# Kernel tuning notes

Hardware: AMD Instinct MI355X
Metric: run time of the kernel (lower is better)

The kernel has to match this reference:

```python
import jax, jax.numpy as jnp
import numpy as np
from functools import partial

N_SEEDS = 1000       # n
BG_LOW, BG_UP = 0.3, 0.7
ERODE_K, ERODE_ITER = 11, 1
KSZ = 3
IGNORE = -255
INT_MAX = np.iinfo(np.int32).max


def _min_pool2d(x, k):
    # binary erosion with a kxk all-ones structuring element, SAME padding
    return jax.lax.reduce_window(x, INT_MAX, jax.lax.min, (k, k), (1, 1), 'SAME')


def _max_pool3d(x, k):
    # binary dilation over (B,H,W) with kxk window on spatial dims
    return jax.lax.reduce_window(x, -INT_MAX, jax.lax.max, (1, k, k), (1, 1, 1), 'SAME')


def _otsu_threshold(flat255):
    # flat255: int32 pixel values in [0,255]
    hist = jnp.zeros(256, jnp.float32).at[flat255].add(1.0)
    total = jnp.asarray(flat255.shape[0], jnp.float32)
    bins = jnp.arange(256, dtype=jnp.float32)
    w = jnp.cumsum(hist)                 # class-0 pixel count up to bin t
    m = jnp.cumsum(hist * bins)          # class-0 intensity mass up to t
    mT = m[-1]
    denom = w * (total - w)
    sigma_b = jnp.where(denom > 0, (mT * w - total * m) ** 2 / (denom * total * total), 0.0)
    th = jnp.argmax(sigma_b).astype(jnp.float32)
    bad = jnp.sum(hist > 0) <= 1         # degenerate histogram -> bad_egg
    return th, bad


def _sample_mask(eligible, key, hw):
    # uniform sampling without replacement of min(N_SEEDS, #eligible)
    # via random-score top-k restricted to eligible positions
    scores = jnp.where(eligible, jax.random.uniform(key, (hw,)), -jnp.inf)
    vals, idx = jax.lax.top_k(scores, N_SEEDS)
    sel = (vals > -jnp.inf).astype(jnp.int32)
    return jnp.zeros(hw, jnp.int32).at[idx].max(sel)


def _one_sample(cam, key):
    h, w = cam.shape
    hw = h * w
    cam255 = jnp.floor(cam * 255.0)
    flat255 = jnp.clip(cam255.astype(jnp.int32).ravel(), 0, 255)

    th, bad = _otsu_threshold(flat255)
    th = jnp.where(bad, jnp.median(cam * 255.0), th)
    th = jnp.where(th == 0, 1.0, jnp.where(th == 255, 254.0, th))

    roi = (cam255 > th).astype(jnp.int32)
    for _ in range(ERODE_ITER):
        roi = _min_pool2d(roi, ERODE_K)

    kf, kb, kz = jax.random.split(key, 3)
    # foreground: sample uniformly from eroded ROI pixels
    fg = _sample_mask(roi.ravel() == 1, kf, hw)
    # background: sample uniformly from the nbr_bg lowest-activation pixels
    z = jax.random.uniform(kz, (), minval=BG_LOW, maxval=BG_UP)
    nbr_bg = jnp.ceil(z * hw)
    order = jnp.argsort(cam.ravel())
    rank = jnp.zeros(hw, jnp.int32).at[order].set(jnp.arange(hw, dtype=jnp.int32))
    bg = _sample_mask(rank.astype(jnp.float32) < nbr_bg, kb, hw)
    return fg.reshape(h, w), bg.reshape(h, w)


def setup_inputs() -> dict:
    key = jax.random.key(0)
    x = jax.random.uniform(key, (128, 1, 512, 512), dtype=jnp.float32)
    return {"x": x}


def reference(x):
    b, d, h, w = x.shape
    keys = jax.random.split(jax.random.key(42), b)
    all_fg, all_bg = jax.vmap(_one_sample)(x[:, 0], keys)   # (B,H,W) int32
    # dilation with ksz x ksz ones kernel
    all_fg = _max_pool3d(all_fg, KSZ)
    all_bg = _max_pool3d(all_bg, KSZ)
    outer = all_fg + all_bg
    all_fg = jnp.where(outer == 2, 0, all_fg)
    all_bg = jnp.where(outer == 2, 0, all_bg)
    out = jnp.full((b, h, w), IGNORE, dtype=jnp.int32)
    out = jnp.where(all_fg == 1, 1, out)
    out = jnp.where(all_bg == 1, 0, out)
    return out
```

## Files before the change

### kernel.cpp

```cpp
#include <hip/hip_runtime.h>
#include <cstdint>

typedef unsigned short u16;

constexpr int BATCH = 128;
constexpr int H = 512, W = 512;
constexpr int HW = H * W;
constexpr int WPR = W / 64;
constexpr int WPI = HW / 64;
constexpr int NSEED = 1000;
constexpr int MARGIN = 3000;
constexpr int CAP2 = 4096;
constexpr int CAPS = 1024;
constexpr int LBUF = 2048;
constexpr int NBIN = 4096;
constexpr int QSEG = 576;

__device__ __forceinline__ uint32_t rotl32(uint32_t v, int d) {
  return (v << d) | (v >> (32 - d));
}

__device__ __forceinline__ void tf2x32(uint32_t k0, uint32_t k1,
                                       uint32_t x0, uint32_t x1,
                                       uint32_t &o0, uint32_t &o1) {
  uint32_t ks2 = k0 ^ k1 ^ 0x1BD11BDAu;
  x0 += k0; x1 += k1;
  x0 += x1; x1 = rotl32(x1, 13); x1 ^= x0;
  x0 += x1; x1 = rotl32(x1, 15); x1 ^= x0;
  x0 += x1; x1 = rotl32(x1, 26); x1 ^= x0;
  x0 += x1; x1 = rotl32(x1, 6);  x1 ^= x0;
  x0 += k1; x1 += ks2 + 1u;
  x0 += x1; x1 = rotl32(x1, 17); x1 ^= x0;
  x0 += x1; x1 = rotl32(x1, 29); x1 ^= x0;
  x0 += x1; x1 = rotl32(x1, 16); x1 ^= x0;
  x0 += x1; x1 = rotl32(x1, 24); x1 ^= x0;
  x0 += ks2; x1 += k0 + 2u;
  x0 += x1; x1 = rotl32(x1, 13); x1 ^= x0;
  x0 += x1; x1 = rotl32(x1, 15); x1 ^= x0;
  x0 += x1; x1 = rotl32(x1, 26); x1 ^= x0;
  x0 += x1; x1 = rotl32(x1, 6);  x1 ^= x0;
  x0 += k0; x1 += k1 + 3u;
  x0 += x1; x1 = rotl32(x1, 17); x1 ^= x0;
  x0 += x1; x1 = rotl32(x1, 29); x1 ^= x0;
  x0 += x1; x1 = rotl32(x1, 16); x1 ^= x0;
  x0 += x1; x1 = rotl32(x1, 24); x1 ^= x0;
  x0 += k1; x1 += ks2 + 4u;
  x0 += x1; x1 = rotl32(x1, 13); x1 ^= x0;
  x0 += x1; x1 = rotl32(x1, 15); x1 ^= x0;
  x0 += x1; x1 = rotl32(x1, 26); x1 ^= x0;
  x0 += x1; x1 = rotl32(x1, 6);  x1 ^= x0;
  x0 += ks2; x1 += k0 + 5u;
  o0 = x0; o1 = x1;
}

__device__ __forceinline__ uint32_t score_bits(uint32_t k0, uint32_t k1, uint32_t i) {
  uint32_t a, c; tf2x32(k0, k1, 0u, i, a, c);
  return a ^ c;
}

__device__ __forceinline__ void keygen(int b, uint32_t* keys, uint32_t* kbg,
                                       uint32_t* Tbg) {
  uint32_t kb0, kb1; tf2x32(0u, 42u, 0u, (uint32_t)b, kb0, kb1);
  uint32_t kf0, kf1; tf2x32(kb0, kb1, 0u, 0u, kf0, kf1);
  uint32_t kB0, kB1; tf2x32(kb0, kb1, 0u, 1u, kB0, kB1);
  uint32_t kz0, kz1; tf2x32(kb0, kb1, 0u, 2u, kz0, kz1);
  uint32_t za, zc; tf2x32(kz0, kz1, 0u, 0u, za, zc);
  uint32_t zb = za ^ zc;
  keys[b * 4 + 0] = kf0; keys[b * 4 + 1] = kf1;
  keys[b * 4 + 2] = kB0; keys[b * 4 + 3] = kB1;
  float uu = __uint_as_float((zb >> 9) | 0x3f800000u) - 1.0f;
  float span = __fsub_rn(0.7f, 0.3f);
  float z = __fadd_rn(__fmul_rn(uu, span), 0.3f);
  z = fmaxf(0.3f, z);
  float nb = ceilf(__fmul_rn(z, (float)HW));
  uint32_t K = (uint32_t)nb;
  kbg[b] = K;
  float tv = floorf((1.0f - (float)MARGIN / (float)K) * 8388608.0f);
  Tbg[b] = (uint32_t)fmaxf(tv, 0.0f);
}

__global__ __launch_bounds__(1024) void k_binify(const float4* __restrict__ x4,
                                                 u16* __restrict__ g,
                                                 uint32_t* __restrict__ gh,
                                                 uint32_t* __restrict__ keys,
                                                 uint32_t* __restrict__ kbg,
                                                 uint32_t* __restrict__ Tbg,
                                                 uint32_t* __restrict__ Efg,
                                                 uint32_t* __restrict__ cnt_fg,
                                                 uint32_t* __restrict__ cnt_be,
                                                 uint32_t* __restrict__ cnt_bg) {
  __shared__ uint32_t h[NBIN];
  int b = blockIdx.x >> 2, sub = blockIdx.x & 3, t = threadIdx.x;
  if (blockIdx.x == 0 && t < BATCH) {
    keygen(t, keys, kbg, Tbg);
    Efg[t] = 0; cnt_fg[t] = 0; cnt_be[t] = 0; cnt_bg[t] = 0;
  }
  for (int i = t; i < NBIN; i += 1024) h[i] = 0;
  __syncthreads();
  const float4* xb = x4 + ((size_t)b * HW + (size_t)sub * (HW / 4)) / 4;
  ushort4* gb4 = (ushort4*)g + ((size_t)b * HW + (size_t)sub * (HW / 4)) / 4;
  for (int i = t; i < HW / 16; i += 1024) {
    float4 v4 = xb[i];
    int g0 = (int)floorf(__fmul_rn(v4.x, 4080.0f)); g0 = min(max(g0, 0), 4079);
    int g1 = (int)floorf(__fmul_rn(v4.y, 4080.0f)); g1 = min(max(g1, 0), 4079);
    int g2 = (int)floorf(__fmul_rn(v4.z, 4080.0f)); g2 = min(max(g2, 0), 4079);
    int g3 = (int)floorf(__fmul_rn(v4.w, 4080.0f)); g3 = min(max(g3, 0), 4079);
    atomicAdd(&h[g0], 1u);
    atomicAdd(&h[g1], 1u);
    atomicAdd(&h[g2], 1u);
    atomicAdd(&h[g3], 1u);
    ushort4 o;
    o.x = (u16)g0; o.y = (u16)g1; o.z = (u16)g2; o.w = (u16)g3;
    gb4[i] = o;
  }
  __syncthreads();
  uint32_t* dst = gh + ((size_t)blockIdx.x << 12);
  for (int i = t; i < NBIN; i += 1024) dst[i] = h[i];
}

__device__ __forceinline__ void lds_tree_cumsum256(float* L, float* S, int tid) {
  const int off[9] = {0, 256, 384, 448, 480, 496, 504, 508, 510};
  const int sz[9]  = {256, 128, 64, 32, 16, 8, 4, 2, 1};
  for (int l = 0; l < 8; ++l) {
    int o = off[l], on = off[l + 1], n = sz[l + 1];
    if (tid < n) L[on + tid] = __fadd_rn(L[o + 2 * tid], L[o + 2 * tid + 1]);
    __syncthreads();
  }
  if (tid == 0) S[off[8]] = L[off[8]];
  __syncthreads();
  for (int l = 7; l >= 0; --l) {
    int o = off[l], on = off[l + 1], hn = sz[l] / 2;
    if (tid == 0) S[o] = L[o];
    if (tid < hn) S[o + 2 * tid + 1] = S[on + tid];
    if (tid >= 1 && tid < hn) S[o + 2 * tid] = __fadd_rn(S[on + tid - 1], L[o + 2 * tid]);
    __syncthreads();
  }
}

__global__ __launch_bounds__(256) void k_otsu_scan(const uint32_t* __restrict__ gh,
                                                   const uint32_t* __restrict__ Ka,
                                                   int* __restrict__ th_out,
                                                   uint32_t* __restrict__ b1a,
                                                   uint32_t* __restrict__ r1a) {
  __shared__ float L[511], S[511], wc[256], mm[256];
  __shared__ float sv[256];
  __shared__ int si[256];
  __shared__ uint32_t h[NBIN];
  __shared__ uint32_t ps[256];
  int tid = threadIdx.x;
  int b = (blockIdx.x < BATCH) ? blockIdx.x : (blockIdx.x - BATCH);
  const uint32_t* g0 = gh + ((size_t)(b * 4 + 0) << 12);
  const uint32_t* g1 = gh + ((size_t)(b * 4 + 1) << 12);
  const uint32_t* g2 = gh + ((size_t)(b * 4 + 2) << 12);
  const uint32_t* g3 = gh + ((size_t)(b * 4 + 3) << 12);
  for (int i = tid; i < NBIN; i += 256) h[i] = g0[i] + g1[i] + g2[i] + g3[i];
  __syncthreads();
  if (blockIdx.x < BATCH) {
    uint32_t hv = 0;
#pragma unroll
    for (int i = 0; i < 16; ++i) hv += h[tid * 16 + i];
    L[tid] = (float)hv;
    __syncthreads();
    lds_tree_cumsum256(L, S, tid);
    wc[tid] = S[tid];
    __syncthreads();
    L[tid] = __fmul_rn((float)hv, (float)tid);
    __syncthreads();
    lds_tree_cumsum256(L, S, tid);
    mm[tid] = S[tid];
    __syncthreads();
    float total = (float)HW;
    float mT = mm[255];
    {
      float w = wc[tid];
      float denom = __fmul_rn(w, __fsub_rn(total, w));
      float s = 0.0f;
      if (denom > 0.0f) {
        float d  = __fsub_rn(__fmul_rn(mT, w), __fmul_rn(total, mm[tid]));
        float nu = __fmul_rn(d, d);
        float dd = __fmul_rn(__fmul_rn(denom, total), total);
        s = __fdiv_rn(nu, dd);
      }
      sv[tid] = s; si[tid] = tid;
    }
    __syncthreads();
    for (int st = 128; st >= 1; st >>= 1) {
      if (tid < st) {
        float s2 = sv[tid + st]; int i2 = si[tid + st];
        if (s2 > sv[tid] || (s2 == sv[tid] && i2 < si[tid])) { sv[tid] = s2; si[tid] = i2; }
      }
      __syncthreads();
    }
    if (tid == 0) {
      int bi = si[0];
      if (bi == 0) bi = 1;
      if (bi == 255) bi = 254;
      th_out[b] = bi;
    }
  } else {
    uint32_t K = Ka[b];
    uint32_t s = 0;
#pragma unroll
    for (int i = 0; i < 16; ++i) s += h[tid * 16 + i];
    ps[tid] = s;
    __syncthreads();
    if (tid == 0) {
      uint32_t acc = 0, b1 = 0, r1 = 1;
      for (int c = 0; c < 256; ++c) {
        if (acc + ps[c] >= K) {
          for (int bin = c * 16; bin < c * 16 + 16; ++bin) {
            uint32_t cc = h[bin];
            if (acc + cc >= K) { b1 = (uint32_t)bin; r1 = K - acc; break; }
            acc += cc;
          }
          break;
        }
        acc += ps[c];
      }
      b1a[b] = b1; r1a[b] = r1;
    }
  }
}

__global__ __launch_bounds__(1024) void k_main(const u16* __restrict__ gq,
                                               const float* __restrict__ x,
                                               const int* __restrict__ th,
                                               const uint32_t* __restrict__ b1a,
                                               const uint32_t* __restrict__ Tbg,
                                               const uint32_t* __restrict__ keys,
                                               uint32_t* __restrict__ Efg,
                                               uint32_t* __restrict__ cnt_bg,
                                               uint64_t* __restrict__ list,
                                               uint32_t* __restrict__ cnt_be,
                                               uint64_t* __restrict__ list_be,
                                               uint64_t* __restrict__ erod) {
  __shared__ uint64_t sroi[1104];
  __shared__ uint64_t srow[1104];
  __shared__ uint32_t wq[16 * QSEG];
  __shared__ uint64_t lbuf[LBUF];
  __shared__ uint32_t lcnt, gbase;
  int b = blockIdx.x >> 2, sub = blockIdx.x & 3, t = threadIdx.x;
  int wave = t >> 6, lane = t & 63;
  int R0 = sub * 128;
  int rlo = max(R0 - 5, 0), rhi = min(R0 + 133, H);
  int nwords = (rhi - rlo) * 8;
  const u16* gb = gq + (size_t)b * HW;
  const float* xb = x + (size_t)b * HW;
  int groi = (th[b] + 1) << 4;
  uint32_t b1 = b1a[b];
  uint32_t T = Tbg[b];
  uint32_t k0 = keys[b * 4 + 2], k1 = keys[b * 4 + 3];
  if (t == 0) lcnt = 0;
  __syncthreads();
  uint32_t* q = wq + wave * QSEG;
  uint32_t qlen = 0, hd = 0;
  uint64_t lmask = (1ull << lane) - 1ull;
  for (int r = 0; r < 8; ++r) {
    int absr = R0 + wave * 8 + r;
    int rowbase = absr * W + lane;
    int swbase = (absr - rlo) * 8;
    const u16* gp8 = gb + rowbase;
    u16 gvals[8];
#pragma unroll
    for (int c = 0; c < 8; ++c) gvals[c] = gp8[c * 64];
#pragma unroll
    for (int c = 0; c < 8; ++c) {
      uint32_t gv = (uint32_t)gvals[c];
      uint64_t bw = __ballot((int)gv >= groi);
      if (lane == 0) sroi[swbase + c] = bw;
      bool elig = gv < b1;
      uint64_t m = __ballot(elig);
      if (elig) {
        uint32_t rank = (uint32_t)__popcll(m & lmask);
        uint32_t idx = hd + qlen + rank;
        if (idx >= (uint32_t)QSEG) idx -= (uint32_t)QSEG;
        q[idx] = (uint32_t)(rowbase + c * 64);
      }
      qlen += (uint32_t)__popcll(m);
      if (gv == b1) {
        uint32_t gp = atomicAdd(&cnt_be[b], 1u);
        if (gp < (uint32_t)CAPS)
          list_be[(size_t)b * CAPS + gp] =
              (((uint64_t)__float_as_uint(xb[rowbase + c * 64])) << 18) |
              (uint32_t)(rowbase + c * 64);
      }
    }
    while (qlen >= 64u) {
      __builtin_amdgcn_wave_barrier();
      uint32_t idx = hd + (uint32_t)lane;
      if (idx >= (uint32_t)QSEG) idx -= (uint32_t)QSEG;
      uint32_t p = q[idx];
      hd += 64u; if (hd >= (uint32_t)QSEG) hd -= (uint32_t)QSEG;
      qlen -= 64u;
      uint32_t v = score_bits(k0, k1, p) >> 9;
      if (v >= T) {
        uint32_t pos = atomicAdd(&lcnt, 1u);
        uint64_t key = (((uint64_t)((~v) & 0x7FFFFFu)) << 18) | p;
        if (pos < (uint32_t)LBUF) lbuf[pos] = key;
        else { uint32_t gp = atomicAdd(&cnt_bg[b], 1u);
               if (gp < (uint32_t)CAP2) list[(size_t)b * CAP2 + gp] = key; }
      }
    }
  }
  if (qlen) {
    __builtin_amdgcn_wave_barrier();
    if ((uint32_t)lane < qlen) {
      uint32_t idx = hd + (uint32_t)lane;
      if (idx >= (uint32_t)QSEG) idx -= (uint32_t)QSEG;
      uint32_t p = q[idx];
      uint32_t v = score_bits(k0, k1, p) >> 9;
      if (v >= T) {
        uint32_t pos = atomicAdd(&lcnt, 1u);
        uint64_t key = (((uint64_t)((~v) & 0x7FFFFFu)) << 18) | p;
        if (pos < (uint32_t)LBUF) lbuf[pos] = key;
        else { uint32_t gp = atomicAdd(&cnt_bg[b], 1u);
               if (gp < (uint32_t)CAP2) list[(size_t)b * CAP2 + gp] = key; }
      }
    }
  }
  {
    int lowWords = (R0 - rlo) * 8;
    int nh = nwords - 1024;
    for (int i = wave; i < nh; i += 16) {
      int wi = i + ((i < lowWords) ? 0 : 1024);
      int absr = rlo + (wi >> 3);
      int c = wi & 7;
      uint32_t gv = (uint32_t)gb[absr * W + c * 64 + lane];
      uint64_t bw = __ballot((int)gv >= groi);
      if (lane == 0) sroi[wi] = bw;
    }
  }
  __syncthreads();
  for (int wi = t; wi < nwords; wi += 1024) {
    int c = wi & 7;
    uint64_t cur = sroi[wi];
    uint64_t left  = (c > 0) ? sroi[wi - 1] : ~0ull;
    uint64_t right = (c < 7) ? sroi[wi + 1] : ~0ull;
    uint64_t res = cur;
#pragma unroll
    for (int s = 1; s <= 5; ++s) {
      res &= (cur >> s) | (right << (64 - s));
      res &= (cur << s) | (left >> (64 - s));
    }
    srow[wi] = res;
  }
  __syncthreads();
  {
    int coreRow = t >> 3, c = t & 7;
    int absr = R0 + coreRow;
    int s = absr - rlo;
    uint64_t res = srow[s * 8 + c];
#pragma unroll
    for (int d = 1; d <= 5; ++d) {
      if (absr - d >= 0) res &= srow[(s - d) * 8 + c];
      if (absr + d < H)  res &= srow[(s + d) * 8 + c];
    }
    erod[(size_t)b * WPI + absr * 8 + c] = res;
    uint32_t pc = (uint32_t)__popcll(res);
    for (int sh = 32; sh >= 1; sh >>= 1) pc += __shfl_down(pc, sh);
    if (lane == 0 && pc) atomicAdd(&Efg[b], pc);
  }
  __syncthreads();
  int m = min((int)lcnt, LBUF);
  if (t == 0) gbase = atomicAdd(&cnt_bg[b], (uint32_t)m);
  __syncthreads();
  uint32_t base = gbase;
  for (int i = t; i < m; i += 1024) {
    uint32_t pos = base + (uint32_t)i;
    if (pos < (uint32_t)CAP2) list[(size_t)b * CAP2 + pos] = lbuf[i];
  }
}

__global__ __launch_bounds__(1024) void k_select(const uint32_t* __restrict__ r1a,
                                                 const uint32_t* __restrict__ cnt_be,
                                                 const uint64_t* __restrict__ list_be,
                                                 const uint32_t* __restrict__ Tbg,
                                                 const uint32_t* __restrict__ keys,
                                                 const uint32_t* __restrict__ cnt_bg,
                                                 const uint64_t* __restrict__ list,
                                                 uint64_t* __restrict__ bmG,
                                                 const uint32_t* __restrict__ Ea,
                                                 uint32_t* __restrict__ cnt_fg,
                                                 uint64_t* __restrict__ list_fg,
                                                 const uint64_t* __restrict__ bmE,
                                                 uint64_t* __restrict__ bmF) {
  __shared__ uint64_t pool[5248];
  __shared__ uint32_t ecnt, tcnt, lcnt, gbase, sb2, sr2;
  int t = threadIdx.x;
  uint32_t* h = (uint32_t*)(pool + 2048);
  uint64_t* tie = pool + 4096;
  uint32_t* S = (uint32_t*)(pool + 5120);
  if (blockIdx.x < BATCH) {
    int b = blockIdx.x;
    uint64_t* ks = pool;
    uint64_t* ebuf = pool + 1024;
    uint64_t* bg = bmG + (size_t)b * WPI;
    for (int i = t; i < WPI; i += 1024) bg[i] = 0;
    int nbe = min((int)cnt_be[b], CAPS);
    if (t == 0) { ecnt = 0; tcnt = 0; }
    if (t < nbe) ks[t] = list_be[(size_t)b * CAPS + t];
    __syncthreads();
    if (t < nbe) {
      uint64_t mk = ks[t];
      int rank = 0;
      for (int i = 0; i < nbe; ++i) rank += (ks[i] < mk) ? 1 : 0;
      int r = min((int)r1a[b], nbe);
      if (rank < r) {
        uint32_t p = (uint32_t)(mk & 0x3FFFFull);
        uint32_t v = score_bits(keys[b * 4 + 2], keys[b * 4 + 3], p) >> 9;
        if (v >= Tbg[b]) {
          uint32_t slot = atomicAdd(&ecnt, 1u);
          ebuf[slot] = (((uint64_t)((~v) & 0x7FFFFFu)) << 18) | p;
        }
      }
    }
    for (int i = t; i < 4096; i += 1024) h[i] = 0;
    __syncthreads();
    int n0 = min((int)cnt_bg[b], CAP2);
    int ne = (int)ecnt;
    int n = n0 + ne;
    if (n == 0) return;
    uint32_t target = (uint32_t)min(NSEED, n);
    const uint64_t* lb = list + (size_t)b * CAP2;
    uint64_t K0 = (t < n0)        ? lb[t]        : 0;
    uint64_t K1 = (t + 1024 < n0) ? lb[t + 1024] : 0;
    uint64_t K2 = (t + 2048 < n0) ? lb[t + 2048] : 0;
    uint64_t K3 = (t + 3072 < n0) ? lb[t + 3072] : 0;
    uint64_t KE = (t < ne)        ? ebuf[t]      : 0;
    if (t < n0)        atomicAdd(&h[(uint32_t)(K0 >> 29)], 1u);
    if (t + 1024 < n0) atomicAdd(&h[(uint32_t)(K1 >> 29)], 1u);
    if (t + 2048 < n0) atomicAdd(&h[(uint32_t)(K2 >> 29)], 1u);
    if (t + 3072 < n0) atomicAdd(&h[(uint32_t)(K3 >> 29)], 1u);
    if (t < ne)        atomicAdd(&h[(uint32_t)(KE >> 29)], 1u);
    __syncthreads();
    if (t < 256) {
      uint32_t s = 0;
#pragma unroll
      for (int i = 0; i < 16; ++i) s += h[t * 16 + i];
      S[t] = s;
    }
    __syncthreads();
    for (int st = 1; st < 256; st <<= 1) {
      uint32_t v = 0;
      if (t < 256 && t >= st) v = S[t - st];
      __syncthreads();
      if (t < 256) S[t] += v;
      __syncthreads();
    }
    if (t < 256) {
      uint32_t before = (t == 0) ? 0u : S[t - 1];
      if (S[t] >= target && before < target) {
        uint32_t acc = before;
        for (int i = 0; i < 16; ++i) {
          uint32_t c = h[t * 16 + i];
          if (acc + c >= target) { sb2 = (uint32_t)(t * 16 + i); sr2 = target - acc; break; }
          acc += c;
        }
      }
    }
    __syncthreads();
    uint32_t b2 = sb2, r2 = sr2;
#define PROC(KK, VALID) \
    if (VALID) { \
      uint32_t bin = (uint32_t)((KK) >> 29); \
      if (bin < b2) { \
        uint32_t p = (uint32_t)(KK) & 0x3FFFFu; \
        atomicOr((unsigned long long*)&bg[p >> 6], 1ull << (p & 63)); \
      } else if (bin == b2) { \
        uint32_t pos = atomicAdd(&tcnt, 1u); \
        if (pos < 1024u) tie[pos] = (KK); \
      } \
    }
    PROC(K0, t < n0) PROC(K1, t + 1024 < n0) PROC(K2, t + 2048 < n0)
    PROC(K3, t + 3072 < n0) PROC(KE, t < ne)
#undef PROC
    __syncthreads();
    int m = min((int)tcnt, 1024);
    int r = min((int)r2, m);
    if (t < m) {
      uint64_t mk = tie[t];
      int rank = 0;
      for (int i = 0; i < m; ++i) rank += (tie[i] < mk) ? 1 : 0;
      if (rank < r) {
        uint32_t p = (uint32_t)mk & 0x3FFFFu;
        atomicOr((unsigned long long*)&bg[p >> 6], 1ull << (p & 63));
      }
    }
  } else {
    int b = blockIdx.x - BATCH;
    uint32_t E = Ea[b];
    if (E <= (uint32_t)NSEED) return;
    uint64_t* lbuf = pool;
    const uint64_t* eb = bmE + (size_t)b * WPI;
    uint64_t* ob = bmF + (size_t)b * WPI;
    for (int i = t; i < WPI; i += 1024) ob[i] = 0;
    if (t == 0) { lcnt = 0; tcnt = 0; }
    __syncthreads();
    float tvf = floorf((1.0f - (float)MARGIN / (float)E) * 8388608.0f);
    uint32_t T = (uint32_t)fmaxf(tvf, 0.0f);
    uint32_t k0 = keys[b * 4 + 0], k1 = keys[b * 4 + 1];
    int lane = t & 63;
    for (int k = 0; k < HW / 1024; ++k) {
      uint32_t p = (uint32_t)(k * 1024 + t);
      uint64_t wbits = eb[p >> 6];
      if ((wbits >> lane) & 1ull) {
        uint32_t v = score_bits(k0, k1, p) >> 9;
        if (v >= T) {
          uint32_t pos = atomicAdd(&lcnt, 1u);
          uint64_t key = (((uint64_t)((~v) & 0x7FFFFFu)) << 18) | p;
          if (pos < (uint32_t)LBUF) lbuf[pos] = key;
          else { uint32_t gp = atomicAdd(&cnt_fg[b], 1u);
                 if (gp < (uint32_t)CAP2) list_fg[(size_t)b * CAP2 + gp] = key; }
        }
      }
    }
    __syncthreads();
    int m2 = min((int)lcnt, LBUF);
    if (t == 0) gbase = atomicAdd(&cnt_fg[b], (uint32_t)m2);
    __syncthreads();
    for (int i = t; i < m2; i += 1024) {
      uint32_t pos = gbase + (uint32_t)i;
      if (pos < (uint32_t)CAP2) list_fg[(size_t)b * CAP2 + pos] = lbuf[i];
    }
    __syncthreads();
    int n = min((int)cnt_fg[b], CAP2);
    if (n == 0) return;
    uint32_t target = (uint32_t)min(NSEED, n);
    const uint64_t* lb = list_fg + (size_t)b * CAP2;
    uint64_t K0 = (t < n)        ? lb[t]        : 0;
    uint64_t K1 = (t + 1024 < n) ? lb[t + 1024] : 0;
    uint64_t K2 = (t + 2048 < n) ? lb[t + 2048] : 0;
    uint64_t K3 = (t + 3072 < n) ? lb[t + 3072] : 0;
    for (int i = t; i < 4096; i += 1024) h[i] = 0;
    __syncthreads();
    if (t < n)        atomicAdd(&h[(uint32_t)(K0 >> 29)], 1u);
    if (t + 1024 < n) atomicAdd(&h[(uint32_t)(K1 >> 29)], 1u);
    if (t + 2048 < n) atomicAdd(&h[(uint32_t)(K2 >> 29)], 1u);
    if (t + 3072 < n) atomicAdd(&h[(uint32_t)(K3 >> 29)], 1u);
    __syncthreads();
    if (t < 256) {
      uint32_t s = 0;
#pragma unroll
      for (int i = 0; i < 16; ++i) s += h[t * 16 + i];
      S[t] = s;
    }
    __syncthreads();
    for (int st = 1; st < 256; st <<= 1) {
      uint32_t v = 0;
      if (t < 256 && t >= st) v = S[t - st];
      __syncthreads();
      if (t < 256) S[t] += v;
      __syncthreads();
    }
    if (t < 256) {
      uint32_t before = (t == 0) ? 0u : S[t - 1];
      if (S[t] >= target && before < target) {
        uint32_t acc = before;
        for (int i = 0; i < 16; ++i) {
          uint32_t c = h[t * 16 + i];
          if (acc + c >= target) { sb2 = (uint32_t)(t * 16 + i); sr2 = target - acc; break; }
          acc += c;
        }
      }
    }
    __syncthreads();
    uint32_t b2 = sb2, r2 = sr2;
#define PROC(KK, VALID) \
    if (VALID) { \
      uint32_t bin = (uint32_t)((KK) >> 29); \
      if (bin < b2) { \
        uint32_t p = (uint32_t)(KK) & 0x3FFFFu; \
        atomicOr((unsigned long long*)&ob[p >> 6], 1ull << (p & 63)); \
      } else if (bin == b2) { \
        uint32_t pos = atomicAdd(&tcnt, 1u); \
        if (pos < 1024u) tie[pos] = (KK); \
      } \
    }
    PROC(K0, t < n) PROC(K1, t + 1024 < n) PROC(K2, t + 2048 < n) PROC(K3, t + 3072 < n)
#undef PROC
    __syncthreads();
    int m = min((int)tcnt, 1024);
    int r = min((int)r2, m);
    if (t < m) {
      uint64_t mk = tie[t];
      int rank = 0;
      for (int i = 0; i < m; ++i) rank += (tie[i] < mk) ? 1 : 0;
      if (rank < r) {
        uint32_t p = (uint32_t)mk & 0x3FFFFu;
        atomicOr((unsigned long long*)&ob[p >> 6], 1ull << (p & 63));
      }
    }
  }
}

__global__ __launch_bounds__(256) void k_compose4(const uint64_t* __restrict__ bmE,
                                                  const uint64_t* __restrict__ bmF,
                                                  const uint64_t* __restrict__ G,
                                                  const uint32_t* __restrict__ Ea,
                                                  int* __restrict__ out) {
  int tid = blockIdx.x * 256 + threadIdx.x;
  int w = tid >> 4;
  int sub = tid & 15;
  int iw = w & (WPI - 1);
  int b = w >> 12;
  const uint64_t* F = (Ea[b] <= (uint32_t)NSEED) ? bmE : bmF;
  int r = iw >> 3, c = iw & 7;
  int ib = w - iw;
  uint64_t Fd = 0, Bd = 0;
#pragma unroll
  for (int dr = -1; dr <= 1; ++dr) {
    int rr = r + dr;
    if (rr < 0 || rr >= H) continue;
    int wi = ib + rr * 8 + c;
    uint64_t cf = F[wi], cg = G[wi];
    uint64_t lf = (c > 0) ? F[wi - 1] : 0ull, lg = (c > 0) ? G[wi - 1] : 0ull;
    uint64_t rf = (c < 7) ? F[wi + 1] : 0ull, rg = (c < 7) ? G[wi + 1] : 0ull;
    Fd |= cf | (cf << 1) | (lf >> 63) | (cf >> 1) | (rf << 63);
    Bd |= cg | (cg << 1) | (lg >> 63) | (cg >> 1) | (rg << 63);
  }
  uint64_t ov = Fd & Bd;
  Fd &= ~ov; Bd &= ~ov;
  int sh = sub * 4;
  int4 o;
  o.x = ((Fd >> (sh + 0)) & 1ull) ? 1 : (((Bd >> (sh + 0)) & 1ull) ? 0 : -255);
  o.y = ((Fd >> (sh + 1)) & 1ull) ? 1 : (((Bd >> (sh + 1)) & 1ull) ? 0 : -255);
  o.z = ((Fd >> (sh + 2)) & 1ull) ? 1 : (((Bd >> (sh + 2)) & 1ull) ? 0 : -255);
  o.w = ((Fd >> (sh + 3)) & 1ull) ? 1 : (((Bd >> (sh + 3)) & 1ull) ? 0 : -255);
  ((int4*)out)[tid] = o;
}

extern "C" void kernel_launch(void* const* d_in, const int* in_sizes, int n_in,
                              void* d_out, int out_size, void* d_ws, size_t ws_size,
                              hipStream_t stream) {
  (void)in_sizes; (void)n_in; (void)out_size; (void)ws_size;
  const float* x = (const float*)d_in[0];
  int* out = (int*)d_out;
  char* ws = (char*)d_ws;

  u16* g = (u16*)d_out;

  uint32_t* keys   = (uint32_t*)(ws + 0);
  uint32_t* kbg    = (uint32_t*)(ws + 2048);
  int*      th     = (int*)     (ws + 2560);
  uint32_t* b1be   = (uint32_t*)(ws + 3072);
  uint32_t* r1be   = (uint32_t*)(ws + 3584);
  uint32_t* Tbg    = (uint32_t*)(ws + 4096);
  uint32_t* Efg    = (uint32_t*)(ws + 4608);
  uint32_t* cnt_fg = (uint32_t*)(ws + 5120);
  uint32_t* cnt_be = (uint32_t*)(ws + 5632);
  uint32_t* cnt_bg = (uint32_t*)(ws + 6144);
  char* P = ws + 8192;
  uint32_t* gh      = (uint32_t*)(P);
  uint64_t* bmG     = (uint64_t*)(P + 8396800 - 8192);
  uint64_t* _bmG    = (uint64_t*)(ws + 8192 + 8388608);
  uint64_t* list    = (uint64_t*)(ws + 8192 + 8388608 + 4194304);
  uint64_t* list_be = (uint64_t*)(ws + 8192 + 8388608 + 8388608);
  uint64_t* bmE     = (uint64_t*)(ws + 8192 + 8388608 + 9437184);
  uint64_t* bmF     = (uint64_t*)(ws + 8192 + 8388608 + 13631488);
  uint64_t* list_fg = (uint64_t*)gh;
  (void)bmG;

  k_binify   <<<BATCH * 4, 1024, 0, stream>>>((const float4*)x, g, gh, keys, kbg,
                                              Tbg, Efg, cnt_fg, cnt_be, cnt_bg);
  k_otsu_scan<<<BATCH * 2, 256, 0, stream>>>(gh, kbg, th, b1be, r1be);
  k_main     <<<BATCH * 4, 1024, 0, stream>>>(g, x, th, b1be, Tbg, keys,
                                              Efg, cnt_bg, list, cnt_be, list_be, bmE);
  k_select   <<<BATCH * 2, 1024, 0, stream>>>(r1be, cnt_be, list_be, Tbg, keys,
                                              cnt_bg, list, _bmG,
                                              Efg, cnt_fg, list_fg, bmE, bmF);
  k_compose4 <<<(BATCH * HW / 4) / 256, 256, 0, stream>>>(bmE, bmF, _bmG, Efg, out);
}
```

Before: 388.8 us.

## Fuse Otsu/background-scan into main kernel and stage dilation bitmaps in LDS

Removes the separate k_otsu_scan launch. Each k_main block now sums the four partial histograms, computes the Otsu threshold and the background bin cutoff itself, and keeps them in LDS through a union that shares space with the ROI buffers. This gets rid of one kernel launch and the global round trip for the threshold values, at the cost of every one of the four sub-blocks per image repeating the histogram work. Separately, the compose kernel now computes the dilated F/B words once per 8-row group into shared memory and writes the outputs from there. Before, every output thread reloaded up to nine bitmap words.

```diff
diff --git a/kernel.cpp b/kernel.cpp
--- a/kernel.cpp
+++ b/kernel.cpp
@@ -137,121 +137,120 @@
   }
 }
 
-__global__ __launch_bounds__(256) void k_otsu_scan(const uint32_t* __restrict__ gh,
-                                                   const uint32_t* __restrict__ Ka,
-                                                   int* __restrict__ th_out,
-                                                   uint32_t* __restrict__ b1a,
-                                                   uint32_t* __restrict__ r1a) {
-  __shared__ float L[511], S[511], wc[256], mm[256];
-  __shared__ float sv[256];
-  __shared__ int si[256];
-  __shared__ uint32_t h[NBIN];
-  __shared__ uint32_t ps[256];
-  int tid = threadIdx.x;
-  int b = (blockIdx.x < BATCH) ? blockIdx.x : (blockIdx.x - BATCH);
-  const uint32_t* g0 = gh + ((size_t)(b * 4 + 0) << 12);
-  const uint32_t* g1 = gh + ((size_t)(b * 4 + 1) << 12);
-  const uint32_t* g2 = gh + ((size_t)(b * 4 + 2) << 12);
-  const uint32_t* g3 = gh + ((size_t)(b * 4 + 3) << 12);
-  for (int i = tid; i < NBIN; i += 256) h[i] = g0[i] + g1[i] + g2[i] + g3[i];
-  __syncthreads();
-  if (blockIdx.x < BATCH) {
-    uint32_t hv = 0;
-#pragma unroll
-    for (int i = 0; i < 16; ++i) hv += h[tid * 16 + i];
-    L[tid] = (float)hv;
-    __syncthreads();
-    lds_tree_cumsum256(L, S, tid);
-    wc[tid] = S[tid];
-    __syncthreads();
-    L[tid] = __fmul_rn((float)hv, (float)tid);
-    __syncthreads();
-    lds_tree_cumsum256(L, S, tid);
-    mm[tid] = S[tid];
-    __syncthreads();
-    float total = (float)HW;
-    float mT = mm[255];
-    {
-      float w = wc[tid];
-      float denom = __fmul_rn(w, __fsub_rn(total, w));
-      float s = 0.0f;
-      if (denom > 0.0f) {
-        float d  = __fsub_rn(__fmul_rn(mT, w), __fmul_rn(total, mm[tid]));
-        float nu = __fmul_rn(d, d);
-        float dd = __fmul_rn(__fmul_rn(denom, total), total);
-        s = __fdiv_rn(nu, dd);
-      }
-      sv[tid] = s; si[tid] = tid;
-    }
-    __syncthreads();
-    for (int st = 128; st >= 1; st >>= 1) {
-      if (tid < st) {
-        float s2 = sv[tid + st]; int i2 = si[tid + st];
-        if (s2 > sv[tid] || (s2 == sv[tid] && i2 < si[tid])) { sv[tid] = s2; si[tid] = i2; }
-      }
-      __syncthreads();
-    }
-    if (tid == 0) {
-      int bi = si[0];
-      if (bi == 0) bi = 1;
-      if (bi == 255) bi = 254;
-      th_out[b] = bi;
-    }
-  } else {
-    uint32_t K = Ka[b];
-    uint32_t s = 0;
-#pragma unroll
-    for (int i = 0; i < 16; ++i) s += h[tid * 16 + i];
-    ps[tid] = s;
-    __syncthreads();
-    if (tid == 0) {
-      uint32_t acc = 0, b1 = 0, r1 = 1;
-      for (int c = 0; c < 256; ++c) {
-        if (acc + ps[c] >= K) {
-          for (int bin = c * 16; bin < c * 16 + 16; ++bin) {
-            uint32_t cc = h[bin];
-            if (acc + cc >= K) { b1 = (uint32_t)bin; r1 = K - acc; break; }
-            acc += cc;
-          }
-          break;
-        }
-        acc += ps[c];
-      }
-      b1a[b] = b1; r1a[b] = r1;
-    }
-  }
-}
-
 __global__ __launch_bounds__(1024) void k_main(const u16* __restrict__ gq,
                                                const float* __restrict__ x,
-                                               const int* __restrict__ th,
-                                               const uint32_t* __restrict__ b1a,
+                                               const uint32_t* __restrict__ gh,
+                                               const uint32_t* __restrict__ kbg,
                                                const uint32_t* __restrict__ Tbg,
                                                const uint32_t* __restrict__ keys,
+                                               uint32_t* __restrict__ r1a,
                                                uint32_t* __restrict__ Efg,
                                                uint32_t* __restrict__ cnt_bg,
                                                uint64_t* __restrict__ list,
                                                uint32_t* __restrict__ cnt_be,
                                                uint64_t* __restrict__ list_be,
                                                uint64_t* __restrict__ erod) {
-  __shared__ uint64_t sroi[1104];
-  __shared__ uint64_t srow[1104];
+  __shared__ union {
+    struct { uint64_t sroi[1104]; uint64_t srow[1104]; } m;
+    struct { uint32_t h[NBIN]; float L[511]; float S[511];
+             float wc[256]; float mm[256]; float sv[256];
+             int si[256]; uint32_t ps[256]; } o;
+  } u;
   __shared__ uint32_t wq[16 * QSEG];
   __shared__ uint64_t lbuf[LBUF];
   __shared__ uint32_t lcnt, gbase;
+  __shared__ int thS;
+  __shared__ uint32_t b1S;
   int b = blockIdx.x >> 2, sub = blockIdx.x & 3, t = threadIdx.x;
   int wave = t >> 6, lane = t & 63;
+
+  {
+    const uint32_t* g0 = gh + ((size_t)(b * 4 + 0) << 12);
+    const uint32_t* g1 = gh + ((size_t)(b * 4 + 1) << 12);
+    const uint32_t* g2 = gh + ((size_t)(b * 4 + 2) << 12);
+    const uint32_t* g3 = gh + ((size_t)(b * 4 + 3) << 12);
+    for (int i = t; i < NBIN; i += 1024) u.o.h[i] = g0[i] + g1[i] + g2[i] + g3[i];
+    __syncthreads();
+    uint32_t hv = 0;
+    if (t < 256) {
+#pragma unroll
+      for (int i = 0; i < 16; ++i) hv += u.o.h[t * 16 + i];
+      u.o.L[t] = (float)hv;
+    }
+    __syncthreads();
+    lds_tree_cumsum256(u.o.L, u.o.S, t);
+    if (t < 256) u.o.wc[t] = u.o.S[t];
+    __syncthreads();
+    if (t < 256) u.o.L[t] = __fmul_rn((float)hv, (float)t);
+    __syncthreads();
+    lds_tree_cumsum256(u.o.L, u.o.S, t);
+    if (t < 256) u.o.mm[t] = u.o.S[t];
+    __syncthreads();
+    if (t < 256) {
+      float total = (float)HW;
+      float mT = u.o.mm[255];
+      float w = u.o.wc[t];
+      float denom = __fmul_rn(w, __fsub_rn(total, w));
+      float s = 0.0f;
+      if (denom > 0.0f) {
+        float d  = __fsub_rn(__fmul_rn(mT, w), __fmul_rn(total, u.o.mm[t]));
+        float nu = __fmul_rn(d, d);
+        float dd = __fmul_rn(__fmul_rn(denom, total), total);
+        s = __fdiv_rn(nu, dd);
+      }
+      u.o.sv[t] = s; u.o.si[t] = t;
+    }
+    __syncthreads();
+    for (int st = 128; st >= 1; st >>= 1) {
+      if (t < st) {
+        float s2 = u.o.sv[t + st]; int i2 = u.o.si[t + st];
+        if (s2 > u.o.sv[t] || (s2 == u.o.sv[t] && i2 < u.o.si[t])) {
+          u.o.sv[t] = s2; u.o.si[t] = i2;
+        }
+      }
+      __syncthreads();
+    }
+    if (t < 256) {
+      uint32_t s = 0;
+#pragma unroll
+      for (int i = 0; i < 16; ++i) s += u.o.h[t * 16 + i];
+      u.o.ps[t] = s;
+    }
+    __syncthreads();
+    if (t == 0) {
+      int bi = u.o.si[0];
+      if (bi == 0) bi = 1;
+      if (bi == 255) bi = 254;
+      thS = bi;
+      uint32_t K = kbg[b];
+      uint32_t acc = 0, b1 = 0, r1 = 1;
+      for (int c = 0; c < 256; ++c) {
+        if (acc + u.o.ps[c] >= K) {
+          for (int bin = c * 16; bin < c * 16 + 16; ++bin) {
+            uint32_t cc = u.o.h[bin];
+            if (acc + cc >= K) { b1 = (uint32_t)bin; r1 = K - acc; break; }
+            acc += cc;
+          }
+          break;
+        }
+        acc += u.o.ps[c];
+      }
+      b1S = b1;
+      if (sub == 0) r1a[b] = r1;
+      lcnt = 0;
+    }
+    __syncthreads();
+  }
+
   int R0 = sub * 128;
   int rlo = max(R0 - 5, 0), rhi = min(R0 + 133, H);
   int nwords = (rhi - rlo) * 8;
   const u16* gb = gq + (size_t)b * HW;
   const float* xb = x + (size_t)b * HW;
-  int groi = (th[b] + 1) << 4;
-  uint32_t b1 = b1a[b];
+  int groi = (thS + 1) << 4;
+  uint32_t b1 = b1S;
   uint32_t T = Tbg[b];
   uint32_t k0 = keys[b * 4 + 2], k1 = keys[b * 4 + 3];
-  if (t == 0) lcnt = 0;
-  __syncthreads();
   uint32_t* q = wq + wave * QSEG;
   uint32_t qlen = 0, hd = 0;
   uint64_t lmask = (1ull << lane) - 1ull;
@@ -267,7 +266,7 @@
     for (int c = 0; c < 8; ++c) {
       uint32_t gv = (uint32_t)gvals[c];
       uint64_t bw = __ballot((int)gv >= groi);
-      if (lane == 0) sroi[swbase + c] = bw;
+      if (lane == 0) u.m.sroi[swbase + c] = bw;
       bool elig = gv < b1;
       uint64_t m = __ballot(elig);
       if (elig) {
@@ -327,33 +326,33 @@
       int c = wi & 7;
       uint32_t gv = (uint32_t)gb[absr * W + c * 64 + lane];
       uint64_t bw = __ballot((int)gv >= groi);
-      if (lane == 0) sroi[wi] = bw;
+      if (lane == 0) u.m.sroi[wi] = bw;
     }
   }
   __syncthreads();
   for (int wi = t; wi < nwords; wi += 1024) {
     int c = wi & 7;
-    uint64_t cur = sroi[wi];
-    uint64_t left  = (c > 0) ? sroi[wi - 1] : ~0ull;
-    uint64_t right = (c < 7) ? sroi[wi + 1] : ~0ull;
+    uint64_t cur = u.m.sroi[wi];
+    uint64_t left  = (c > 0) ? u.m.sroi[wi - 1] : ~0ull;
+    uint64_t right = (c < 7) ? u.m.sroi[wi + 1] : ~0ull;
     uint64_t res = cur;
 #pragma unroll
     for (int s = 1; s <= 5; ++s) {
       res &= (cur >> s) | (right << (64 - s));
       res &= (cur << s) | (left >> (64 - s));
     }
-    srow[wi] = res;
+    u.m.srow[wi] = res;
   }
   __syncthreads();
   {
     int coreRow = t >> 3, c = t & 7;
     int absr = R0 + coreRow;
     int s = absr - rlo;
-    uint64_t res = srow[s * 8 + c];
+    uint64_t res = u.m.srow[s * 8 + c];
 #pragma unroll
     for (int d = 1; d <= 5; ++d) {
-      if (absr - d >= 0) res &= srow[(s - d) * 8 + c];
-      if (absr + d < H)  res &= srow[(s + d) * 8 + c];
+      if (absr - d >= 0) res &= u.m.srow[(s - d) * 8 + c];
+      if (absr + d < H)  res &= u.m.srow[(s + d) * 8 + c];
     }
     erod[(size_t)b * WPI + absr * 8 + c] = res;
     uint32_t pc = (uint32_t)__popcll(res);
@@ -593,40 +592,50 @@
   }
 }
 
-__global__ __launch_bounds__(256) void k_compose4(const uint64_t* __restrict__ bmE,
+__global__ __launch_bounds__(256) void k_compose2(const uint64_t* __restrict__ bmE,
                                                   const uint64_t* __restrict__ bmF,
                                                   const uint64_t* __restrict__ G,
                                                   const uint32_t* __restrict__ Ea,
                                                   int* __restrict__ out) {
-  int tid = blockIdx.x * 256 + threadIdx.x;
-  int w = tid >> 4;
-  int sub = tid & 15;
-  int iw = w & (WPI - 1);
-  int b = w >> 12;
-  const uint64_t* F = (Ea[b] <= (uint32_t)NSEED) ? bmE : bmF;
-  int r = iw >> 3, c = iw & 7;
-  int ib = w - iw;
-  uint64_t Fd = 0, Bd = 0;
-#pragma unroll
-  for (int dr = -1; dr <= 1; ++dr) {
-    int rr = r + dr;
-    if (rr < 0 || rr >= H) continue;
-    int wi = ib + rr * 8 + c;
-    uint64_t cf = F[wi], cg = G[wi];
-    uint64_t lf = (c > 0) ? F[wi - 1] : 0ull, lg = (c > 0) ? G[wi - 1] : 0ull;
-    uint64_t rf = (c < 7) ? F[wi + 1] : 0ull, rg = (c < 7) ? G[wi + 1] : 0ull;
-    Fd |= cf | (cf << 1) | (lf >> 63) | (cf >> 1) | (rf << 63);
-    Bd |= cg | (cg << 1) | (lg >> 63) | (cg >> 1) | (rg << 63);
-  }
-  uint64_t ov = Fd & Bd;
-  Fd &= ~ov; Bd &= ~ov;
-  int sh = sub * 4;
-  int4 o;
-  o.x = ((Fd >> (sh + 0)) & 1ull) ? 1 : (((Bd >> (sh + 0)) & 1ull) ? 0 : -255);
-  o.y = ((Fd >> (sh + 1)) & 1ull) ? 1 : (((Bd >> (sh + 1)) & 1ull) ? 0 : -255);
-  o.z = ((Fd >> (sh + 2)) & 1ull) ? 1 : (((Bd >> (sh + 2)) & 1ull) ? 0 : -255);
-  o.w = ((Fd >> (sh + 3)) & 1ull) ? 1 : (((Bd >> (sh + 3)) & 1ull) ? 0 : -255);
-  ((int4*)out)[tid] = o;
+  __shared__ uint64_t FdS[64], BdS[64];
+  int blk = blockIdx.x;
+  int b = blk >> 6, rg = blk & 63;
+  int t = threadIdx.x;
+  const uint64_t* Fsrc = (Ea[b] <= (uint32_t)NSEED) ? bmE : bmF;
+  const uint64_t* Fb = Fsrc + (size_t)b * WPI;
+  const uint64_t* Gb = G + (size_t)b * WPI;
+  if (t < 128) {
+    const uint64_t* src = (t < 64) ? Fb : Gb;
+    int w = t & 63;
+    int r = rg * 8 + (w >> 3), c = w & 7;
+    uint64_t d = 0;
+#pragma unroll
+    for (int dr = -1; dr <= 1; ++dr) {
+      int rr = r + dr;
+      if (rr < 0 || rr >= H) continue;
+      int wi = rr * 8 + c;
+      uint64_t cur = src[wi];
+      uint64_t lf = (c > 0) ? src[wi - 1] : 0ull;
+      uint64_t rt = (c < 7) ? src[wi + 1] : 0ull;
+      d |= cur | (cur << 1) | (lf >> 63) | (cur >> 1) | (rt << 63);
+    }
+    if (t < 64) FdS[w] = d; else BdS[w] = d;
+  }
+  __syncthreads();
+  int4* ob = (int4*)out + ((size_t)b * HW + (size_t)rg * 4096) / 4;
+  for (int i = t; i < 1024; i += 256) {
+    int w = i >> 4, sub = i & 15;
+    uint64_t Fd = FdS[w], Bd = BdS[w];
+    uint64_t ov = Fd & Bd;
+    Fd &= ~ov; Bd &= ~ov;
+    int sh = sub * 4;
+    int4 o;
+    o.x = ((Fd >> (sh + 0)) & 1ull) ? 1 : (((Bd >> (sh + 0)) & 1ull) ? 0 : -255);
+    o.y = ((Fd >> (sh + 1)) & 1ull) ? 1 : (((Bd >> (sh + 1)) & 1ull) ? 0 : -255);
+    o.z = ((Fd >> (sh + 2)) & 1ull) ? 1 : (((Bd >> (sh + 2)) & 1ull) ? 0 : -255);
+    o.w = ((Fd >> (sh + 3)) & 1ull) ? 1 : (((Bd >> (sh + 3)) & 1ull) ? 0 : -255);
+    ob[i] = o;
+  }
 }
 
 extern "C" void kernel_launch(void* const* d_in, const int* in_sizes, int n_in,
@@ -641,32 +650,26 @@
 
   uint32_t* keys   = (uint32_t*)(ws + 0);
   uint32_t* kbg    = (uint32_t*)(ws + 2048);
-  int*      th     = (int*)     (ws + 2560);
-  uint32_t* b1be   = (uint32_t*)(ws + 3072);
-  uint32_t* r1be   = (uint32_t*)(ws + 3584);
+  uint32_t* r1a    = (uint32_t*)(ws + 3584);
   uint32_t* Tbg    = (uint32_t*)(ws + 4096);
   uint32_t* Efg    = (uint32_t*)(ws + 4608);
   uint32_t* cnt_fg = (uint32_t*)(ws + 5120);
   uint32_t* cnt_be = (uint32_t*)(ws + 5632);
   uint32_t* cnt_bg = (uint32_t*)(ws + 6144);
-  char* P = ws + 8192;
-  uint32_t* gh      = (uint32_t*)(P);
-  uint64_t* bmG     = (uint64_t*)(P + 8396800 - 8192);
-  uint64_t* _bmG    = (uint64_t*)(ws + 8192 + 8388608);
+  uint32_t* gh      = (uint32_t*)(ws + 8192);
+  uint64_t* bmG     = (uint64_t*)(ws + 8192 + 8388608);
   uint64_t* list    = (uint64_t*)(ws + 8192 + 8388608 + 4194304);
   uint64_t* list_be = (uint64_t*)(ws + 8192 + 8388608 + 8388608);
   uint64_t* bmE     = (uint64_t*)(ws + 8192 + 8388608 + 9437184);
   uint64_t* bmF     = (uint64_t*)(ws + 8192 + 8388608 + 13631488);
   uint64_t* list_fg = (uint64_t*)gh;
-  (void)bmG;
 
   k_binify   <<<BATCH * 4, 1024, 0, stream>>>((const float4*)x, g, gh, keys, kbg,
                                               Tbg, Efg, cnt_fg, cnt_be, cnt_bg);
-  k_otsu_scan<<<BATCH * 2, 256, 0, stream>>>(gh, kbg, th, b1be, r1be);
-  k_main     <<<BATCH * 4, 1024, 0, stream>>>(g, x, th, b1be, Tbg, keys,
+  k_main     <<<BATCH * 4, 1024, 0, stream>>>(g, x, gh, kbg, Tbg, keys, r1a,
                                               Efg, cnt_bg, list, cnt_be, list_be, bmE);
-  k_select   <<<BATCH * 2, 1024, 0, stream>>>(r1be, cnt_be, list_be, Tbg, keys,
-                                              cnt_bg, list, _bmG,
+  k_select   <<<BATCH * 2, 1024, 0, stream>>>(r1a, cnt_be, list_be, Tbg, keys,
+                                              cnt_bg, list, bmG,
                                               Efg, cnt_fg, list_fg, bmE, bmF);
-  k_compose4 <<<(BATCH * HW / 4) / 256, 256, 0, stream>>>(bmE, bmF, _bmG, Efg, out);
-}
+  k_compose2 <<<BATCH * 64, 256, 0, stream>>>(bmE, bmF, bmG, Efg, out);
+}
```

New measurement: 379.0 us. -2.5%, faster.
